# Kernel optimization log

Measured on AMD Instinct MI355X. Metric: run time of the kernel, lower is better.

The kernel has to match this reference:

```python
import jax, jax.numpy as jnp
import numpy as np
import math

B, S, D, H = 2, 2048, 1024, 16
DK = D // H


def setup_inputs() -> dict:
    key = jax.random.key(0)
    ks = jax.random.split(key, 8)
    scale = 0.02
    f = lambda k, shape: jax.random.normal(k, shape, dtype=jnp.float32)
    causal = jnp.tril(jnp.ones((S, S), dtype=jnp.int32))  # [S,S]
    mask = jnp.broadcast_to(causal[None, None], (B, 1, S, S))
    return {
        "query": f(ks[0], (B, S, D)),
        "key_in": f(ks[1], (B, S, D)),
        "value": f(ks[2], (B, S, D)),
        "Wq": f(ks[3], (D, D)) * scale, "bq": jnp.zeros((D,), jnp.float32),
        "Wk": f(ks[4], (D, D)) * scale, "bk": jnp.zeros((D,), jnp.float32),
        "Wv": f(ks[5], (D, D)) * scale, "bv": jnp.zeros((D,), jnp.float32),
        "Wo": f(ks[6], (D, D)) * scale, "bo": jnp.zeros((D,), jnp.float32),
        "mask": mask,
    }


def reference(query, key_in, value, Wq, bq, Wk, bk, Wv, bv, Wo, bo, mask):
    # linear projections (torch Linear: x @ W.T + b), split into heads -> [B,H,S,DK]
    def proj(x, W, b):
        return (x @ W.T + b).reshape(B, -1, H, DK).transpose(0, 2, 1, 3)

    q = proj(query, Wq, bq)
    k = proj(key_in, Wk, bk)
    v = proj(value, Wv, bv)

    scores = jnp.einsum("bhqd,bhkd->bhqk", q, k) / math.sqrt(DK)  # [B,H,S,S]
    scores = jnp.where(mask.astype(bool), scores, -jnp.inf)
    attn = jax.nn.softmax(scores, axis=-1)
    x = jnp.einsum("bhqk,bhkd->bhqd", attn, v)  # [B,H,S,DK]
    x = x.transpose(0, 2, 1, 3).reshape(B, S, D)
    return x @ Wo.T + bo
```

## Files before the change

kernel.cpp:

```cpp
#include <hip/hip_runtime.h>
#include <hip/hip_bf16.h>

constexpr int Bc = 2, Sc = 2048, Dc = 1024, Hc = 16, DKc = 64;
constexpr int Nrows = Bc * Sc;

typedef short bf16x8 __attribute__((ext_vector_type(8)));
typedef short bf16x4 __attribute__((ext_vector_type(4)));
typedef float floatx4 __attribute__((ext_vector_type(4)));
typedef unsigned short u16x8 __attribute__((ext_vector_type(8)));

__device__ __forceinline__ short f2bf(float f) {
    union { float f; unsigned u; } v; v.f = f;
    unsigned r = v.u + 0x7FFFu + ((v.u >> 16) & 1u);
    return (short)(r >> 16);
}

__device__ __forceinline__ void gld16(const void* g, void* l) {
    __builtin_amdgcn_global_load_lds((const __attribute__((address_space(1))) unsigned int*)g,
                                     (__attribute__((address_space(3))) unsigned int*)l,
                                     16, 0, 0);
}

__global__ __launch_bounds__(256) void cvt_bf16(
        const float* __restrict__ s0, const float* __restrict__ s1, const float* __restrict__ s2,
        const float* __restrict__ s3, const float* __restrict__ s4, const float* __restrict__ s5,
        const float* __restrict__ s6,
        short* __restrict__ d0, short* __restrict__ d1, short* __restrict__ d2,
        short* __restrict__ d3, short* __restrict__ d4, short* __restrict__ d5,
        short* __restrict__ d6) {
    const float* src; short* dst; int n;
    switch (blockIdx.y) {
        case 0: src = s0; dst = d0; n = Nrows * Dc; break;
        case 1: src = s1; dst = d1; n = Nrows * Dc; break;
        case 2: src = s2; dst = d2; n = Nrows * Dc; break;
        case 3: src = s3; dst = d3; n = Dc * Dc; break;
        case 4: src = s4; dst = d4; n = Dc * Dc; break;
        case 5: src = s5; dst = d5; n = Dc * Dc; break;
        default: src = s6; dst = d6; n = Dc * Dc; break;
    }
    const int stride = gridDim.x * 256 * 8;
    for (int i = (blockIdx.x * 256 + threadIdx.x) * 8; i < n; i += stride) {
        const float4 a = *(const float4*)(src + i);
        const float4 b = *(const float4*)(src + i + 4);
        u16x8 o;
        o[0] = (unsigned short)f2bf(a.x); o[1] = (unsigned short)f2bf(a.y);
        o[2] = (unsigned short)f2bf(a.z); o[3] = (unsigned short)f2bf(a.w);
        o[4] = (unsigned short)f2bf(b.x); o[5] = (unsigned short)f2bf(b.y);
        o[6] = (unsigned short)f2bf(b.z); o[7] = (unsigned short)f2bf(b.w);
        *(u16x8*)(dst + i) = o;
    }
}

template <int BM>
__device__ __forceinline__ void gemm_body(const short* __restrict__ A,
                                          const short* __restrict__ W,
                                          const float* __restrict__ bias,
                                          void* __restrict__ Cout,
                                          int mode, short* As, short* Ws) {
    constexpr int K = Dc, BK = 64;
    constexpr int MB = BM / 16;
    constexpr int A_BLKS = MB * 2;
    constexpr int TOT = A_BLKS + 16;
    constexpr int PER_W = TOT / 4;
    constexpr int WMB = MB / 2;

    const int tid  = threadIdx.x;
    const int w    = tid >> 6;
    const int lane = tid & 63;
    const int quad = lane >> 4;
    const int l15  = lane & 15;
    const int rowBase = blockIdx.y * BM;
    const int colBase = blockIdx.x * 128;
    const int wm = w >> 1, wn = w & 1;

    floatx4 acc[WMB][4];
#pragma unroll
    for (int j = 0; j < WMB; ++j)
#pragma unroll
        for (int t = 0; t < 4; ++t) acc[j][t] = (floatx4){0.f, 0.f, 0.f, 0.f};

    for (int k0 = 0; k0 < K; k0 += BK) {
        __syncthreads();
#pragma unroll
        for (int i = 0; i < PER_W; ++i) {
            const int blk = w * PER_W + i;
            if (blk < A_BLKS) {
                const int mb = blk >> 1, kh = blk & 1;
                const short* g = A + (size_t)(rowBase + mb * 16 + l15) * K + k0 + kh * 32 + quad * 8;
                gld16(g, As + blk * 512);
            } else {
                const int b2 = blk - A_BLKS;
                const int nb = b2 >> 1, kh = b2 & 1;
                const short* g = W + (size_t)(colBase + nb * 16 + l15) * K + k0 + kh * 32 + quad * 8;
                gld16(g, Ws + b2 * 512);
            }
        }
        __syncthreads();

        bf16x8 af[WMB][2], wf[4][2];
#pragma unroll
        for (int j = 0; j < WMB; ++j)
#pragma unroll
            for (int kh = 0; kh < 2; ++kh)
                af[j][kh] = *(const bf16x8*)(As + ((wm * WMB + j) * 2 + kh) * 512 + lane * 8);
#pragma unroll
        for (int t = 0; t < 4; ++t)
#pragma unroll
            for (int kh = 0; kh < 2; ++kh)
                wf[t][kh] = *(const bf16x8*)(Ws + ((wn * 4 + t) * 2 + kh) * 512 + lane * 8);

#pragma unroll
        for (int kh = 0; kh < 2; ++kh)
#pragma unroll
            for (int j = 0; j < WMB; ++j)
#pragma unroll
                for (int t = 0; t < 4; ++t)
                    acc[j][t] = __builtin_amdgcn_mfma_f32_16x16x32_bf16(af[j][kh], wf[t][kh], acc[j][t], 0, 0, 0);
    }

#pragma unroll
    for (int j = 0; j < WMB; ++j) {
#pragma unroll
        for (int t = 0; t < 4; ++t) {
            const int col = colBase + wn * 64 + t * 16 + l15;
            const float bv = bias[col];
            const int row0 = rowBase + (wm * WMB + j) * 16 + quad * 4;
            if (mode == 0) {
                float* Co = (float*)Cout;
#pragma unroll
                for (int r = 0; r < 4; ++r)
                    Co[(size_t)(row0 + r) * Dc + col] = acc[j][t][r] + bv;
            } else {
                short* Co = (short*)Cout;
                const int b = row0 >> 11;
                const int ss0 = row0 & (Sc - 1);
                const int h = col >> 6, dk = col & 63;
                if (mode == 1) {
#pragma unroll
                    for (int r = 0; r < 4; ++r)
                        Co[(((size_t)(b * Hc + h)) * Sc + ss0 + r) * DKc + dk] = f2bf(acc[j][t][r] + bv);
                } else {
                    short4 pk;
                    pk.x = f2bf(acc[j][t][0] + bv); pk.y = f2bf(acc[j][t][1] + bv);
                    pk.z = f2bf(acc[j][t][2] + bv); pk.w = f2bf(acc[j][t][3] + bv);
                    *(short4*)(Co + (((size_t)(b * Hc + h)) * DKc + dk) * Sc + ss0) = pk;
                }
            }
        }
    }
}

__global__ __launch_bounds__(256) void gemm_qkv(
        const short* __restrict__ Aq, const short* __restrict__ Ak, const short* __restrict__ Av,
        const short* __restrict__ Wq, const short* __restrict__ Wk, const short* __restrict__ Wv,
        const float* __restrict__ bq, const float* __restrict__ bk, const float* __restrict__ bv,
        short* __restrict__ Oq, short* __restrict__ Ok, short* __restrict__ Ov) {
    __shared__ short As[128 * 64];
    __shared__ short Ws[128 * 64];
    const int z = blockIdx.z;
    const short* A = (z == 0) ? Aq : (z == 1) ? Ak : Av;
    const short* W = (z == 0) ? Wq : (z == 1) ? Wk : Wv;
    const float* bs = (z == 0) ? bq : (z == 1) ? bk : bv;
    short* O = (z == 0) ? Oq : (z == 1) ? Ok : Ov;
    gemm_body<128>(A, W, bs, O, (z == 2) ? 2 : 1, As, Ws);
}

__global__ __launch_bounds__(256) void gemm_out(const short* __restrict__ A,
                                                const short* __restrict__ W,
                                                const float* __restrict__ bias,
                                                float* __restrict__ C) {
    __shared__ short As[64 * 64];
    __shared__ short Ws[128 * 64];
    gemm_body<64>(A, W, bias, C, 0, As, Ws);
}

__global__ __launch_bounds__(256) void flash_attn_mfma(const short* __restrict__ Qg,
                                                       const short* __restrict__ Kg,
                                                       const short* __restrict__ Vtg,
                                                       short* __restrict__ X) {
    __shared__ short Ks[8 * 512];
    __shared__ short Vs[8 * 512];

    const int bh = blockIdx.x;
    const int yy = blockIdx.y;
    const int qt = (yy & 1) ? (31 - (yy >> 1)) : (yy >> 1);

    const int tid  = threadIdx.x;
    const int w    = tid >> 6;
    const int lane = tid & 63;
    const int quad = lane >> 4;
    const int l15  = lane & 15;

    const short* Qb = Qg  + (size_t)bh * Sc * DKc;
    const short* Kb = Kg  + (size_t)bh * Sc * DKc;
    const short* Vb = Vtg + (size_t)bh * DKc * Sc;

    bf16x8 qf[2];
    {
        const short* qp = Qb + (size_t)(qt * 64 + w * 16 + l15) * DKc + quad * 8;
        qf[0] = *(const bf16x8*)(qp);
        qf[1] = *(const bf16x8*)(qp + 32);
    }

    floatx4 oacc[4];
#pragma unroll
    for (int t = 0; t < 4; ++t) oacc[t] = (floatx4){0.f, 0.f, 0.f, 0.f};
    float m_run = -1e30f, l_run = 0.f;
    const int qloc = w * 16 + l15;

    for (int kt = 0; kt <= qt; ++kt) {
        __syncthreads();
#pragma unroll
        for (int i = 0; i < 4; ++i) {
            const int blk = w * 4 + i;
            if (blk < 8) {
                const int t = blk >> 1, kh = blk & 1;
                gld16(Kb + (size_t)(kt * 64 + t * 16 + l15) * DKc + kh * 32 + quad * 8,
                      Ks + blk * 512);
            } else {
                const int b2 = blk - 8, dt = b2 >> 1, t2 = b2 & 1;
                gld16(Vb + (size_t)(dt * 16 + l15) * Sc + kt * 64 + t2 * 32 + quad * 8,
                      Vs + b2 * 512);
            }
        }
        __syncthreads();

        floatx4 sacc[4];
#pragma unroll
        for (int t = 0; t < 4; ++t) sacc[t] = (floatx4){0.f, 0.f, 0.f, 0.f};
#pragma unroll
        for (int t = 0; t < 4; ++t)
#pragma unroll
            for (int kh = 0; kh < 2; ++kh) {
                const bf16x8 af = *(const bf16x8*)(Ks + (t * 2 + kh) * 512 + lane * 8);
                sacc[t] = __builtin_amdgcn_mfma_f32_16x16x32_bf16(af, qf[kh], sacc[t], 0, 0, 0);
            }

        const bool diag = (kt == qt);
#pragma unroll
        for (int t = 0; t < 4; ++t)
#pragma unroll
            for (int r = 0; r < 4; ++r) {
                float s = sacc[t][r] * 0.125f;
                if (diag && (t * 16 + quad * 4 + r) > qloc) s = -1e30f;
                sacc[t][r] = s;
            }

        float mt = sacc[0][0];
#pragma unroll
        for (int t = 0; t < 4; ++t)
#pragma unroll
            for (int r = 0; r < 4; ++r) mt = fmaxf(mt, sacc[t][r]);
        mt = fmaxf(mt, __shfl_xor(mt, 16));
        mt = fmaxf(mt, __shfl_xor(mt, 32));

        const float mn = fmaxf(m_run, mt);
        const float alpha = __expf(m_run - mn);
        m_run = mn;

        float rs = 0.f;
        bf16x8 pf[4];
#pragma unroll
        for (int t = 0; t < 4; ++t) {
            float p0 = __expf(sacc[t][0] - mn);
            float p1 = __expf(sacc[t][1] - mn);
            float p2 = __expf(sacc[t][2] - mn);
            float p3 = __expf(sacc[t][3] - mn);
            rs += (p0 + p1) + (p2 + p3);
            pf[t][0] = f2bf(p0); pf[t][1] = f2bf(p1);
            pf[t][2] = f2bf(p2); pf[t][3] = f2bf(p3);
            pf[t][4] = 0; pf[t][5] = 0; pf[t][6] = 0; pf[t][7] = 0;
        }
        rs += __shfl_xor(rs, 16);
        rs += __shfl_xor(rs, 32);
        l_run = l_run * alpha + rs;
#pragma unroll
        for (int dt = 0; dt < 4; ++dt) oacc[dt] *= alpha;

#pragma unroll
        for (int t = 0; t < 4; ++t) {
            const int L2 = ((t & 1) * 2 + (quad >> 1)) * 16 + l15;
            const int j0 = (quad & 1) * 4;
#pragma unroll
            for (int dt = 0; dt < 4; ++dt) {
                const bf16x4 vv = *(const bf16x4*)(Vs + (dt * 2 + (t >> 1)) * 512 + L2 * 8 + j0);
                bf16x8 vf;
                vf[0] = vv[0]; vf[1] = vv[1]; vf[2] = vv[2]; vf[3] = vv[3];
                vf[4] = 0; vf[5] = 0; vf[6] = 0; vf[7] = 0;
                oacc[dt] = __builtin_amdgcn_mfma_f32_16x16x32_bf16(vf, pf[t], oacc[dt], 0, 0, 0);
            }
        }
    }

    const float inv = 1.0f / l_run;
    const int b = bh >> 4, h = bh & 15;
    const int qrow = qt * 64 + w * 16 + l15;
    short* Xr = X + ((size_t)b * Sc + qrow) * Dc + h * DKc;
#pragma unroll
    for (int dt = 0; dt < 4; ++dt) {
        short4 pk;
        pk.x = f2bf(oacc[dt][0] * inv);
        pk.y = f2bf(oacc[dt][1] * inv);
        pk.z = f2bf(oacc[dt][2] * inv);
        pk.w = f2bf(oacc[dt][3] * inv);
        *(short4*)(Xr + dt * 16 + quad * 4) = pk;
    }
}

extern "C" void kernel_launch(void* const* d_in, const int* in_sizes, int n_in,
                              void* d_out, int out_size, void* d_ws, size_t ws_size,
                              hipStream_t stream) {
    const float* query  = (const float*)d_in[0];
    const float* key_in = (const float*)d_in[1];
    const float* value  = (const float*)d_in[2];
    const float* Wq = (const float*)d_in[3];
    const float* bq = (const float*)d_in[4];
    const float* Wk = (const float*)d_in[5];
    const float* bk = (const float*)d_in[6];
    const float* Wv = (const float*)d_in[7];
    const float* bv = (const float*)d_in[8];
    const float* Wo = (const float*)d_in[9];
    const float* bo = (const float*)d_in[10];

    constexpr size_t TEN = (size_t)Nrows * Dc;
    constexpr size_t WTEN = (size_t)Dc * Dc;
    short* qbf = (short*)d_ws;
    short* kbf = qbf + TEN;
    short* vbf = kbf + TEN;
    short* wqb = vbf + TEN;
    short* wkb = wqb + WTEN;
    short* wvb = wkb + WTEN;
    short* wob = wvb + WTEN;
    short* Qh  = wob + WTEN;
    short* Kh  = Qh + TEN;
    short* Vt  = Kh + TEN;
    short* Xb  = Vt + TEN;

    cvt_bf16<<<dim3(512, 7), 256, 0, stream>>>(query, key_in, value, Wq, Wk, Wv, Wo,
                                               qbf, kbf, vbf, wqb, wkb, wvb, wob);

    gemm_qkv<<<dim3(Dc / 128, Nrows / 128, 3), 256, 0, stream>>>(
        qbf, kbf, vbf, wqb, wkb, wvb, bq, bk, bv, Qh, Kh, Vt);

    flash_attn_mfma<<<dim3(Bc * Hc, Sc / 64), 256, 0, stream>>>(Qh, Kh, Vt, Xb);

    gemm_out<<<dim3(Dc / 128, Nrows / 64), 256, 0, stream>>>(Xb, wob, bo, (float*)d_out);
}
```

Baseline: 303.5 us.

## Double-buffer K/V tiles, fold softmax scale into Q, use full-K PV MFMAs

Q is pre-scaled by 1/sqrt(dk)*log2(e) in the projection epilogue, so the attention loop uses exp2 with no per-element multiply. K/V tiles are now double-buffered, with the next tile's global-to-LDS load issued before the current tile's compute. P is staged through per-wave LDS so the PV product runs as full 32-wide K MFMAs instead of half-zero-padded ones, halving PV MFMA count. The tile schedule drops the interleaving in favor of longest-first order. It adds LDS traffic and a waitcnt, and relies on the global-to-LDS load into the other buffer finishing before the next barrier.

```diff
diff --git a/kernel.cpp b/kernel.cpp
--- a/kernel.cpp
+++ b/kernel.cpp
@@ -3,6 +3,7 @@
 
 constexpr int Bc = 2, Sc = 2048, Dc = 1024, Hc = 16, DKc = 64;
 constexpr int Nrows = Bc * Sc;
+constexpr float QSC = 0.125f * 1.4426950408889634f;
 
 typedef short bf16x8 __attribute__((ext_vector_type(8)));
 typedef short bf16x4 __attribute__((ext_vector_type(4)));
@@ -135,10 +136,11 @@
                 const int b = row0 >> 11;
                 const int ss0 = row0 & (Sc - 1);
                 const int h = col >> 6, dk = col & 63;
-                if (mode == 1) {
+                if (mode == 1 || mode == 3) {
+                    const float sc = (mode == 3) ? QSC : 1.0f;
 #pragma unroll
                     for (int r = 0; r < 4; ++r)
-                        Co[(((size_t)(b * Hc + h)) * Sc + ss0 + r) * DKc + dk] = f2bf(acc[j][t][r] + bv);
+                        Co[(((size_t)(b * Hc + h)) * Sc + ss0 + r) * DKc + dk] = f2bf((acc[j][t][r] + bv) * sc);
                 } else {
                     short4 pk;
                     pk.x = f2bf(acc[j][t][0] + bv); pk.y = f2bf(acc[j][t][1] + bv);
@@ -162,7 +164,7 @@
     const short* W = (z == 0) ? Wq : (z == 1) ? Wk : Wv;
     const float* bs = (z == 0) ? bq : (z == 1) ? bk : bv;
     short* O = (z == 0) ? Oq : (z == 1) ? Ok : Ov;
-    gemm_body<128>(A, W, bs, O, (z == 2) ? 2 : 1, As, Ws);
+    gemm_body<128>(A, W, bs, O, (z == 0) ? 3 : (z == 1) ? 1 : 2, As, Ws);
 }
 
 __global__ __launch_bounds__(256) void gemm_out(const short* __restrict__ A,
@@ -178,12 +180,11 @@
                                                        const short* __restrict__ Kg,
                                                        const short* __restrict__ Vtg,
                                                        short* __restrict__ X) {
-    __shared__ short Ks[8 * 512];
-    __shared__ short Vs[8 * 512];
+    __shared__ short KV[2][16 * 512];
+    __shared__ short Pl[4][16 * 72];
 
     const int bh = blockIdx.x;
-    const int yy = blockIdx.y;
-    const int qt = (yy & 1) ? (31 - (yy >> 1)) : (yy >> 1);
+    const int qt = 31 - blockIdx.y;
 
     const int tid  = threadIdx.x;
     const int w    = tid >> 6;
@@ -202,28 +203,38 @@
         qf[1] = *(const bf16x8*)(qp + 32);
     }
 
-    floatx4 oacc[4];
-#pragma unroll
-    for (int t = 0; t < 4; ++t) oacc[t] = (floatx4){0.f, 0.f, 0.f, 0.f};
-    float m_run = -1e30f, l_run = 0.f;
-    const int qloc = w * 16 + l15;
-
-    for (int kt = 0; kt <= qt; ++kt) {
-        __syncthreads();
+    auto stage = [&](int kt, int buf) {
 #pragma unroll
         for (int i = 0; i < 4; ++i) {
             const int blk = w * 4 + i;
             if (blk < 8) {
                 const int t = blk >> 1, kh = blk & 1;
                 gld16(Kb + (size_t)(kt * 64 + t * 16 + l15) * DKc + kh * 32 + quad * 8,
-                      Ks + blk * 512);
+                      &KV[buf][blk * 512]);
             } else {
-                const int b2 = blk - 8, dt = b2 >> 1, t2 = b2 & 1;
-                gld16(Vb + (size_t)(dt * 16 + l15) * Sc + kt * 64 + t2 * 32 + quad * 8,
-                      Vs + b2 * 512);
-            }
-        }
+                const int b2 = blk - 8, dt = b2 >> 1, kh = b2 & 1;
+                gld16(Vb + (size_t)(dt * 16 + l15) * Sc + kt * 64 + kh * 32 + quad * 8,
+                      &KV[buf][blk * 512]);
+            }
+        }
+    };
+
+    floatx4 oacc[4];
+#pragma unroll
+    for (int t = 0; t < 4; ++t) oacc[t] = (floatx4){0.f, 0.f, 0.f, 0.f};
+    float m_run = -1e30f, l_run = 0.f;
+    const int qloc = w * 16 + l15;
+    short* Pw = &Pl[w][0];
+
+    stage(0, 0);
+
+    for (int kt = 0; kt <= qt; ++kt) {
+        const int cur = kt & 1;
         __syncthreads();
+        if (kt < qt) stage(kt + 1, cur ^ 1);
+
+        const short* Ks = &KV[cur][0];
+        const short* Vs = &KV[cur][8 * 512];
 
         floatx4 sacc[4];
 #pragma unroll
@@ -236,15 +247,13 @@
                 sacc[t] = __builtin_amdgcn_mfma_f32_16x16x32_bf16(af, qf[kh], sacc[t], 0, 0, 0);
             }
 
-        const bool diag = (kt == qt);
-#pragma unroll
-        for (int t = 0; t < 4; ++t)
-#pragma unroll
-            for (int r = 0; r < 4; ++r) {
-                float s = sacc[t][r] * 0.125f;
-                if (diag && (t * 16 + quad * 4 + r) > qloc) s = -1e30f;
-                sacc[t][r] = s;
-            }
+        if (kt == qt) {
+#pragma unroll
+            for (int t = 0; t < 4; ++t)
+#pragma unroll
+                for (int r = 0; r < 4; ++r)
+                    if ((t * 16 + quad * 4 + r) > qloc) sacc[t][r] = -1e30f;
+        }
 
         float mt = sacc[0][0];
 #pragma unroll
@@ -255,21 +264,20 @@
         mt = fmaxf(mt, __shfl_xor(mt, 32));
 
         const float mn = fmaxf(m_run, mt);
-        const float alpha = __expf(m_run - mn);
+        const float alpha = exp2f(m_run - mn);
         m_run = mn;
 
         float rs = 0.f;
-        bf16x8 pf[4];
 #pragma unroll
         for (int t = 0; t < 4; ++t) {
-            float p0 = __expf(sacc[t][0] - mn);
-            float p1 = __expf(sacc[t][1] - mn);
-            float p2 = __expf(sacc[t][2] - mn);
-            float p3 = __expf(sacc[t][3] - mn);
+            const float p0 = exp2f(sacc[t][0] - mn);
+            const float p1 = exp2f(sacc[t][1] - mn);
+            const float p2 = exp2f(sacc[t][2] - mn);
+            const float p3 = exp2f(sacc[t][3] - mn);
             rs += (p0 + p1) + (p2 + p3);
-            pf[t][0] = f2bf(p0); pf[t][1] = f2bf(p1);
-            pf[t][2] = f2bf(p2); pf[t][3] = f2bf(p3);
-            pf[t][4] = 0; pf[t][5] = 0; pf[t][6] = 0; pf[t][7] = 0;
+            bf16x4 pk;
+            pk[0] = f2bf(p0); pk[1] = f2bf(p1); pk[2] = f2bf(p2); pk[3] = f2bf(p3);
+            *(bf16x4*)(Pw + l15 * 72 + t * 16 + quad * 4) = pk;
         }
         rs += __shfl_xor(rs, 16);
         rs += __shfl_xor(rs, 32);
@@ -277,19 +285,19 @@
 #pragma unroll
         for (int dt = 0; dt < 4; ++dt) oacc[dt] *= alpha;
 
-#pragma unroll
-        for (int t = 0; t < 4; ++t) {
-            const int L2 = ((t & 1) * 2 + (quad >> 1)) * 16 + l15;
-            const int j0 = (quad & 1) * 4;
+        __asm__ __volatile__("s_waitcnt lgkmcnt(0)" ::: "memory");
+
+        bf16x8 pb[2];
+#pragma unroll
+        for (int kh = 0; kh < 2; ++kh)
+            pb[kh] = *(const bf16x8*)(Pw + l15 * 72 + kh * 32 + quad * 8);
+#pragma unroll
+        for (int kh = 0; kh < 2; ++kh)
 #pragma unroll
             for (int dt = 0; dt < 4; ++dt) {
-                const bf16x4 vv = *(const bf16x4*)(Vs + (dt * 2 + (t >> 1)) * 512 + L2 * 8 + j0);
-                bf16x8 vf;
-                vf[0] = vv[0]; vf[1] = vv[1]; vf[2] = vv[2]; vf[3] = vv[3];
-                vf[4] = 0; vf[5] = 0; vf[6] = 0; vf[7] = 0;
-                oacc[dt] = __builtin_amdgcn_mfma_f32_16x16x32_bf16(vf, pf[t], oacc[dt], 0, 0, 0);
-            }
-        }
+                const bf16x8 vf = *(const bf16x8*)(Vs + (dt * 2 + kh) * 512 + lane * 8);
+                oacc[dt] = __builtin_amdgcn_mfma_f32_16x16x32_bf16(vf, pb[kh], oacc[dt], 0, 0, 0);
+            }
     }
 
     const float inv = 1.0f / l_run;
```

New measurement: 287.0 us. 5.4% less time.
